# Kernel optimization log

Measured on AMD Instinct MI355X. Metric: run time of the kernel, lower is better.

## Reference

```python
import jax, jax.numpy as jnp
import numpy as np

NUM_BLOCKS_TOTAL = 24  # num_layers(3) * num_blocks(8)
DIL_CYCLE = 8          # dilation = 2 ** (i % 8)


def setup_inputs() -> dict:
    key = jax.random.key(0)
    ks = jax.random.split(key, 12)
    B, C, S, Tq = 256, 32, 32, 256  # batch, residual_ch, skip_ch, queue length
    w = lambda k, sh: jax.random.normal(k, sh, jnp.float32) * 0.1
    return {
        "queues": jax.random.normal(ks[0], (NUM_BLOCKS_TOTAL, B, C, Tq), jnp.float32),
        "x": jax.random.normal(ks[1], (B, 1, 1), jnp.float32),
        "num": jax.random.normal(ks[2], (B, 8, 1), jnp.float32),
        "cat": jax.random.randint(ks[3], (B, 1, 1), 0, 1000),
        "emb_table": w(ks[4], (1000, 16)),
        "W_in": w(ks[5], (C, 25)), "b_in": jnp.zeros((C,), jnp.float32),
        "W_conv": w(ks[6], (NUM_BLOCKS_TOTAL, 2 * C, C, 2)),
        "b_conv": jnp.zeros((NUM_BLOCKS_TOTAL, 2 * C), jnp.float32),
        "W_res": w(ks[7], (NUM_BLOCKS_TOTAL, C, C)),
        "b_res": jnp.zeros((NUM_BLOCKS_TOTAL, C), jnp.float32),
        "W_skip": w(ks[8], (NUM_BLOCKS_TOTAL, S, C)),
        "b_skip": jnp.zeros((NUM_BLOCKS_TOTAL, S), jnp.float32),
        "W_o1": w(ks[9], (128, NUM_BLOCKS_TOTAL * S)), "b_o1": jnp.zeros((128,), jnp.float32),
        "W_o2": w(ks[10], (1, 128)), "b_o2": jnp.zeros((1,), jnp.float32),
    }


def reference(queues, x, num, cat, emb_table, W_in, b_in, W_conv, b_conv,
              W_res, b_res, W_skip, b_skip, W_o1, b_o1, W_o2, b_o2):
    # --- input assembly: concat(x, num, embeds(cat)) along channels, 1 timestep ---
    emb = emb_table[cat[:, 0, 0]][:, :, None]            # [B,16,1]
    inp = jnp.concatenate([x, num, emb], axis=1)          # [B,25,1]
    # pointwise input_conv (kernel_size=1)
    cur = jnp.einsum('oc,bct->bot', W_in, inp) + b_in[None, :, None]  # [B,C,1]

    new_queues = []
    skips = []
    for i in range(NUM_BLOCKS_TOTAL):
        d = 2 ** (i % DIL_CYCLE)
        q = jnp.concatenate([queues[i], cur], axis=2)     # grow queue: [B,C,Tq+1]
        new_queues.append(q)
        # fast_forward: kernel-2 dilated causal conv on last and (last - d) taps
        tap0 = q[:, :, -1 - d]                            # [B,C]
        tap1 = q[:, :, -1]                                # [B,C]
        z = tap0 @ W_conv[i, :, :, 0].T + tap1 @ W_conv[i, :, :, 1].T + b_conv[i]  # [B,2C]
        fz, gz = jnp.split(z, 2, axis=1)
        gated = jnp.tanh(fz) * jax.nn.sigmoid(gz)          # [B,C]
        skips.append(gated @ W_skip[i].T + b_skip[i])      # [B,S]
        cur = (gated @ W_res[i].T + b_res[i] + tap1)[:, :, None]  # residual -> next queue

    sk = jax.nn.relu(jnp.concatenate(skips, axis=1))       # [B, 24*S]
    sk = jax.nn.relu(sk @ W_o1.T + b_o1)                   # [B,128]
    out = (sk @ W_o2.T + b_o2)[:, :, None]                 # [B,1,1]
    return out, jnp.stack(new_queues, axis=0)
```

## Files before the change

### kernel.cpp

```cpp
#include <hip/hip_runtime.h>

#define NBLK 24
#define BATCH 256
#define CCH 32
#define TQ 256
#define TQO 257
#define NCOMP 32
#define BPG 8
#define ROWS_PER_WG 16

__global__ __launch_bounds__(256) void w2w_kernel(
    const float* __restrict__ qin,
    const float* __restrict__ x,
    const float* __restrict__ num,
    const int*   __restrict__ cat,
    const float* __restrict__ emb,
    const float* __restrict__ W_in,  const float* __restrict__ b_in,
    const float* __restrict__ W_conv,const float* __restrict__ b_conv,
    const float* __restrict__ W_res, const float* __restrict__ b_res,
    const float* __restrict__ W_skip,const float* __restrict__ b_skip,
    const float* __restrict__ W_o1,  const float* __restrict__ b_o1,
    const float* __restrict__ W_o2,  const float* __restrict__ b_o2,
    float* __restrict__ out, float* __restrict__ qout)
{
    const int tid = threadIdx.x;

    if (blockIdx.x >= NCOMP) {
        const int wg = blockIdx.x - NCOMP;
        const int row_base = wg * ROWS_PER_WG;
        const int rsub = tid >> 6;
        const int t4   = tid & 63;
        #pragma unroll
        for (int rr = 0; rr < ROWS_PER_WG; rr += 4) {
            const int r = row_base + rr + rsub;
            const float4 v = *(const float4*)(qin + (size_t)r * TQ + t4 * 4);
            float* dst = qout + (size_t)r * TQO + t4 * 4;
            dst[0] = v.x; dst[1] = v.y; dst[2] = v.z; dst[3] = v.w;
        }
        return;
    }

    __shared__ float s_tap[BPG][CCH + 1];
    __shared__ float s_cur[BPG][CCH + 1];
    __shared__ float s_g  [BPG][CCH + 1];
    __shared__ float s_sk [BPG][CCH + 1];

    const int bl = tid >> 5;
    const int j  = tid & 31;
    const int b  = blockIdx.x * BPG + bl;

    float inp[25];
    inp[0] = x[b];
    #pragma unroll
    for (int k = 0; k < 8; ++k) inp[1 + k] = num[b * 8 + k];
    const int ci = cat[b];
    #pragma unroll
    for (int k = 0; k < 16; ++k) inp[9 + k] = emb[ci * 16 + k];

    float cur = b_in[j];
    #pragma unroll
    for (int c = 0; c < 25; ++c) cur = fmaf(W_in[j * 25 + c], inp[c], cur);

    float h0 = 0.f, h1 = 0.f, h2 = 0.f, h3 = 0.f;

    for (int i = 0; i < NBLK; ++i) {
        const int d = 1 << (i & 7);
        const float tap0 = qin[((size_t)(i * BATCH + b) * CCH + j) * TQ + (TQ - d)];

        s_tap[bl][j] = tap0;
        s_cur[bl][j] = cur;
        __syncthreads();

        float z0 = b_conv[i * 2 * CCH + j];
        float z1 = b_conv[i * 2 * CCH + CCH + j];
        const float* wc0 = W_conv + (size_t)(i * 2 * CCH + j)       * CCH * 2;
        const float* wc1 = W_conv + (size_t)(i * 2 * CCH + CCH + j) * CCH * 2;
        #pragma unroll
        for (int c = 0; c < CCH; ++c) {
            const float t0 = s_tap[bl][c];
            const float t1 = s_cur[bl][c];
            z0 = fmaf(t0, wc0[c * 2], z0);
            z0 = fmaf(t1, wc0[c * 2 + 1], z0);
            z1 = fmaf(t0, wc1[c * 2], z1);
            z1 = fmaf(t1, wc1[c * 2 + 1], z1);
        }
        const float g = tanhf(z0) * (1.f / (1.f + __expf(-z1)));

        qout[((size_t)(i * BATCH + b) * CCH + j) * TQO + TQ] = cur;

        s_g[bl][j] = g;
        __syncthreads();

        float sk = b_skip[i * CCH + j];
        float cn = b_res[i * CCH + j] + cur;
        const float* ws = W_skip + (size_t)(i * CCH + j) * CCH;
        const float* wr = W_res  + (size_t)(i * CCH + j) * CCH;
        #pragma unroll
        for (int k = 0; k < CCH; ++k) {
            const float gk = s_g[bl][k];
            sk = fmaf(gk, ws[k], sk);
            cn = fmaf(gk, wr[k], cn);
        }
        s_sk[bl][j] = fmaxf(sk, 0.f);
        cur = cn;
        __syncthreads();

        const float* wo1 = W_o1 + i * CCH;
        #pragma unroll
        for (int s = 0; s < CCH; ++s) {
            const float rs = s_sk[bl][s];
            h0 = fmaf(rs, wo1[(j)      * (NBLK * CCH) + s], h0);
            h1 = fmaf(rs, wo1[(j + 32) * (NBLK * CCH) + s], h1);
            h2 = fmaf(rs, wo1[(j + 64) * (NBLK * CCH) + s], h2);
            h3 = fmaf(rs, wo1[(j + 96) * (NBLK * CCH) + s], h3);
        }
    }

    float p = 0.f;
    p = fmaf(fmaxf(h0 + b_o1[j],      0.f), W_o2[j],      p);
    p = fmaf(fmaxf(h1 + b_o1[j + 32], 0.f), W_o2[j + 32], p);
    p = fmaf(fmaxf(h2 + b_o1[j + 64], 0.f), W_o2[j + 64], p);
    p = fmaf(fmaxf(h3 + b_o1[j + 96], 0.f), W_o2[j + 96], p);
    #pragma unroll
    for (int m = 16; m >= 1; m >>= 1) p += __shfl_xor(p, m);
    if (j == 0) out[b] = p + b_o2[0];
}

extern "C" void kernel_launch(void* const* d_in, const int* in_sizes, int n_in,
                              void* d_out, int out_size, void* d_ws, size_t ws_size,
                              hipStream_t stream) {
    const float* qin    = (const float*)d_in[0];
    const float* x      = (const float*)d_in[1];
    const float* num    = (const float*)d_in[2];
    const int*   cat    = (const int*)  d_in[3];
    const float* emb    = (const float*)d_in[4];
    const float* W_in   = (const float*)d_in[5];
    const float* b_in   = (const float*)d_in[6];
    const float* W_conv = (const float*)d_in[7];
    const float* b_conv = (const float*)d_in[8];
    const float* W_res  = (const float*)d_in[9];
    const float* b_res  = (const float*)d_in[10];
    const float* W_skip = (const float*)d_in[11];
    const float* b_skip = (const float*)d_in[12];
    const float* W_o1   = (const float*)d_in[13];
    const float* b_o1   = (const float*)d_in[14];
    const float* W_o2   = (const float*)d_in[15];
    const float* b_o2   = (const float*)d_in[16];

    float* out  = (float*)d_out;
    float* qout = (float*)d_out + BATCH;

    const int rows  = NBLK * BATCH * CCH;
    const int ncopy = rows / ROWS_PER_WG;
    dim3 grid(NCOMP + ncopy), block(256);
    hipLaunchKernelGGL(w2w_kernel, grid, block, 0, stream,
                       qin, x, num, cat, emb, W_in, b_in, W_conv, b_conv,
                       W_res, b_res, W_skip, b_skip, W_o1, b_o1, W_o2, b_o2,
                       out, qout);
}
```

Measured before the change: 559.0 us.

## Stage per-block weights in LDS with register prefetch and realign queue copy

The compute blocks now prefetch the next layer's conv, residual, skip and output weights into registers and commit them to shared memory, so the FMA loops read vectorized, swizzled LDS instead of strided global loads. Intra-wave barriers replace two of the three block-wide syncs per layer, and the next tap is loaded one layer ahead. The copy path now assigns 16 rows per wave instead of per workgroup, with destination-aligned float4 stores and scalar fixups for edge elements. This raises LDS usage and register pressure, and the copy now uses unaligned vector loads.

```diff
diff --git a/kernel.cpp b/kernel.cpp
--- a/kernel.cpp
+++ b/kernel.cpp
@@ -7,7 +7,11 @@
 #define TQO 257
 #define NCOMP 32
 #define BPG 8
-#define ROWS_PER_WG 16
+#define NCOPY 3072
+#define ROWS (NBLK*BATCH*CCH)
+
+typedef float f4a4  __attribute__((ext_vector_type(4), aligned(4)));
+typedef float f4a16 __attribute__((ext_vector_type(4)));
 
 __global__ __launch_bounds__(256) void w2w_kernel(
     const float* __restrict__ qin,
@@ -23,97 +27,169 @@
     const float* __restrict__ W_o2,  const float* __restrict__ b_o2,
     float* __restrict__ out, float* __restrict__ qout)
 {
+    __shared__ __align__(16) float smem[11264];
     const int tid = threadIdx.x;
 
     if (blockIdx.x >= NCOMP) {
-        const int wg = blockIdx.x - NCOMP;
-        const int row_base = wg * ROWS_PER_WG;
-        const int rsub = tid >> 6;
-        const int t4   = tid & 63;
-        #pragma unroll
-        for (int rr = 0; rr < ROWS_PER_WG; rr += 4) {
-            const int r = row_base + rr + rsub;
-            const float4 v = *(const float4*)(qin + (size_t)r * TQ + t4 * 4);
-            float* dst = qout + (size_t)r * TQO + t4 * 4;
-            dst[0] = v.x; dst[1] = v.y; dst[2] = v.z; dst[3] = v.w;
+        const int wid  = (blockIdx.x - NCOMP) * 4 + (tid >> 6);
+        const int lane = tid & 63;
+        size_t r = (size_t)wid * 16;
+        for (int rr = 0; rr < 16; ++rr, ++r) {
+            const size_t sb = r * TQ, db = r * TQO;
+            const int a = (4 - ((int)r & 3)) & 3;
+            if (lane < 63) {
+                f4a4 v = *(const f4a4*)(qin + sb + a + 4 * lane);
+                *(f4a16*)(qout + db + a + 4 * lane) = v;
+            } else {
+                #pragma unroll
+                for (int e = 0; e < 4; ++e) {
+                    const int f = (e < a) ? e : e + 252;
+                    qout[db + f] = qin[sb + f];
+                }
+            }
         }
         return;
     }
 
-    __shared__ float s_tap[BPG][CCH + 1];
-    __shared__ float s_cur[BPG][CCH + 1];
-    __shared__ float s_g  [BPG][CCH + 1];
-    __shared__ float s_sk [BPG][CCH + 1];
+    float* s_wc = smem;
+    float* s_wr = smem + 4096;
+    float* s_ws = smem + 5120;
+    float* s_wo = smem + 6144;
+    float* s_tc = smem + 10240;
+    float* s_g  = smem + 10752;
+    float* s_sk = smem + 11008;
 
     const int bl = tid >> 5;
     const int j  = tid & 31;
+    const int sw = j & 7;
     const int b  = blockIdx.x * BPG + bl;
 
-    float inp[25];
-    inp[0] = x[b];
-    #pragma unroll
-    for (int k = 0; k < 8; ++k) inp[1 + k] = num[b * 8 + k];
-    const int ci = cat[b];
-    #pragma unroll
-    for (int k = 0; k < 16; ++k) inp[9 + k] = emb[ci * 16 + k];
-
-    float cur = b_in[j];
-    #pragma unroll
-    for (int c = 0; c < 25; ++c) cur = fmaf(W_in[j * 25 + c], inp[c], cur);
+    float cur;
+    {
+        float acc = b_in[j];
+        acc = fmaf(W_in[j * 25 + 0], x[b], acc);
+        #pragma unroll
+        for (int k = 0; k < 8; ++k) acc = fmaf(W_in[j * 25 + 1 + k], num[b * 8 + k], acc);
+        const int ci = cat[b];
+        #pragma unroll
+        for (int k = 0; k < 16; ++k) acc = fmaf(W_in[j * 25 + 9 + k], emb[ci * 16 + k], acc);
+        cur = acc;
+    }
 
     float h0 = 0.f, h1 = 0.f, h2 = 0.f, h3 = 0.f;
+    f4a16 rg[10];
+
+    auto issue = [&](int i) {
+        const float* pc = W_conv + (size_t)i * 4096;
+        #pragma unroll
+        for (int k = 0; k < 4; ++k) rg[k] = *(const f4a16*)(pc + (size_t)(tid + 256 * k) * 4);
+        rg[4] = *(const f4a16*)(W_res  + (size_t)i * 1024 + tid * 4);
+        rg[5] = *(const f4a16*)(W_skip + (size_t)i * 1024 + tid * 4);
+        #pragma unroll
+        for (int k = 0; k < 4; ++k) {
+            const int fi = tid + 256 * k;
+            const int m = fi >> 3, p = fi & 7;
+            rg[6 + k] = *(const f4a16*)(W_o1 + (size_t)m * 768 + (size_t)i * 32 + p * 4);
+        }
+    };
+    auto commit = [&]() {
+        #pragma unroll
+        for (int k = 0; k < 4; ++k) *(f4a16*)(s_wc + (tid + 256 * k) * 4) = rg[k];
+        *(f4a16*)(s_wr + tid * 4) = rg[4];
+        *(f4a16*)(s_ws + tid * 4) = rg[5];
+        #pragma unroll
+        for (int k = 0; k < 4; ++k) *(f4a16*)(s_wo + (tid + 256 * k) * 4) = rg[6 + k];
+    };
+
+    issue(0);
+    {
+        const float t0 = qin[((size_t)b * CCH + j) * TQ + (TQ - 1)];
+        s_tc[bl * 64 + 2 * j]     = t0;
+        s_tc[bl * 64 + 2 * j + 1] = cur;
+    }
+    commit();
+    __syncthreads();
 
     for (int i = 0; i < NBLK; ++i) {
-        const int d = 1 << (i & 7);
-        const float tap0 = qin[((size_t)(i * BATCH + b) * CCH + j) * TQ + (TQ - d)];
-
-        s_tap[bl][j] = tap0;
-        s_cur[bl][j] = cur;
+        if (i + 1 < NBLK) issue(i + 1);
+        float tap_nxt = 0.f;
+        if (i + 1 < NBLK) {
+            const int d = 1 << ((i + 1) & 7);
+            tap_nxt = qin[((size_t)((i + 1) * BATCH + b) * CCH + j) * TQ + (TQ - d)];
+        }
+        const float bc0 = b_conv[i * 64 + j];
+        const float bc1 = b_conv[i * 64 + 32 + j];
+        const float brj = b_res[i * 32 + j];
+        const float bsj = b_skip[i * 32 + j];
+
+        const f4a16* wr0 = (const f4a16*)(s_wc) + j * 16;
+        const f4a16* wr1 = (const f4a16*)(s_wc) + (32 + j) * 16;
+        const f4a16* tcv = (const f4a16*)(s_tc) + bl * 16;
+        float z0a = 0.f, z0b = 0.f, z1a = 0.f, z1b = 0.f;
+        #pragma unroll
+        for (int t = 0; t < 16; ++t) {
+            const int k = (t & 8) | ((t ^ sw) & 7);
+            const f4a16 w0 = wr0[k], w1 = wr1[k], dv = tcv[k];
+            z0a = fmaf(w0.x, dv.x, z0a); z0b = fmaf(w0.y, dv.y, z0b);
+            z0a = fmaf(w0.z, dv.z, z0a); z0b = fmaf(w0.w, dv.w, z0b);
+            z1a = fmaf(w1.x, dv.x, z1a); z1b = fmaf(w1.y, dv.y, z1b);
+            z1a = fmaf(w1.z, dv.z, z1a); z1b = fmaf(w1.w, dv.w, z1b);
+        }
+        const float z0 = z0a + z0b + bc0;
+        const float z1 = z1a + z1b + bc1;
+        const float g  = tanhf(z0) * (1.f / (1.f + __expf(-z1)));
+
+        qout[((size_t)(i * BATCH + b) * CCH + j) * TQO + TQ] = cur;
+
+        s_g[bl * 32 + j] = g;
+        __builtin_amdgcn_wave_barrier();
+
+        const f4a16* gv  = (const f4a16*)(s_g)  + bl * 8;
+        const f4a16* wsv = (const f4a16*)(s_ws) + j * 8;
+        const f4a16* wrv = (const f4a16*)(s_wr) + j * 8;
+        float ska = bsj, skb = 0.f, cna = brj + cur, cnb = 0.f;
+        #pragma unroll
+        for (int t = 0; t < 8; ++t) {
+            const int k = (t ^ sw) & 7;
+            const f4a16 gk = gv[k], wv = wsv[k], rv = wrv[k];
+            ska = fmaf(gk.x, wv.x, ska); skb = fmaf(gk.y, wv.y, skb);
+            ska = fmaf(gk.z, wv.z, ska); skb = fmaf(gk.w, wv.w, skb);
+            cna = fmaf(gk.x, rv.x, cna); cnb = fmaf(gk.y, rv.y, cnb);
+            cna = fmaf(gk.z, rv.z, cna); cnb = fmaf(gk.w, rv.w, cnb);
+        }
+        const float skr = fmaxf(ska + skb, 0.f);
+        cur = cna + cnb;
+
+        s_sk[bl * 32 + j] = skr;
+        if (i + 1 < NBLK) {
+            s_tc[bl * 64 + 2 * j]     = tap_nxt;
+            s_tc[bl * 64 + 2 * j + 1] = cur;
+        }
+        __builtin_amdgcn_wave_barrier();
+
+        const f4a16* skv = (const f4a16*)(s_sk) + bl * 8;
+        const f4a16* o0 = (const f4a16*)(s_wo) + j * 8;
+        const f4a16* o1 = (const f4a16*)(s_wo) + (32 + j) * 8;
+        const f4a16* o2 = (const f4a16*)(s_wo) + (64 + j) * 8;
+        const f4a16* o3 = (const f4a16*)(s_wo) + (96 + j) * 8;
+        #pragma unroll
+        for (int t = 0; t < 8; ++t) {
+            const int k = (t ^ sw) & 7;
+            const f4a16 rv = skv[k];
+            const f4a16 a0 = o0[k], a1 = o1[k], a2 = o2[k], a3 = o3[k];
+            h0 = fmaf(rv.x, a0.x, h0); h0 = fmaf(rv.y, a0.y, h0);
+            h0 = fmaf(rv.z, a0.z, h0); h0 = fmaf(rv.w, a0.w, h0);
+            h1 = fmaf(rv.x, a1.x, h1); h1 = fmaf(rv.y, a1.y, h1);
+            h1 = fmaf(rv.z, a1.z, h1); h1 = fmaf(rv.w, a1.w, h1);
+            h2 = fmaf(rv.x, a2.x, h2); h2 = fmaf(rv.y, a2.y, h2);
+            h2 = fmaf(rv.z, a2.z, h2); h2 = fmaf(rv.w, a2.w, h2);
+            h3 = fmaf(rv.x, a3.x, h3); h3 = fmaf(rv.y, a3.y, h3);
+            h3 = fmaf(rv.z, a3.z, h3); h3 = fmaf(rv.w, a3.w, h3);
+        }
+
         __syncthreads();
-
-        float z0 = b_conv[i * 2 * CCH + j];
-        float z1 = b_conv[i * 2 * CCH + CCH + j];
-        const float* wc0 = W_conv + (size_t)(i * 2 * CCH + j)       * CCH * 2;
-        const float* wc1 = W_conv + (size_t)(i * 2 * CCH + CCH + j) * CCH * 2;
-        #pragma unroll
-        for (int c = 0; c < CCH; ++c) {
-            const float t0 = s_tap[bl][c];
-            const float t1 = s_cur[bl][c];
-            z0 = fmaf(t0, wc0[c * 2], z0);
-            z0 = fmaf(t1, wc0[c * 2 + 1], z0);
-            z1 = fmaf(t0, wc1[c * 2], z1);
-            z1 = fmaf(t1, wc1[c * 2 + 1], z1);
-        }
-        const float g = tanhf(z0) * (1.f / (1.f + __expf(-z1)));
-
-        qout[((size_t)(i * BATCH + b) * CCH + j) * TQO + TQ] = cur;
-
-        s_g[bl][j] = g;
+        if (i + 1 < NBLK) commit();
         __syncthreads();
-
-        float sk = b_skip[i * CCH + j];
-        float cn = b_res[i * CCH + j] + cur;
-        const float* ws = W_skip + (size_t)(i * CCH + j) * CCH;
-        const float* wr = W_res  + (size_t)(i * CCH + j) * CCH;
-        #pragma unroll
-        for (int k = 0; k < CCH; ++k) {
-            const float gk = s_g[bl][k];
-            sk = fmaf(gk, ws[k], sk);
-            cn = fmaf(gk, wr[k], cn);
-        }
-        s_sk[bl][j] = fmaxf(sk, 0.f);
-        cur = cn;
-        __syncthreads();
-
-        const float* wo1 = W_o1 + i * CCH;
-        #pragma unroll
-        for (int s = 0; s < CCH; ++s) {
-            const float rs = s_sk[bl][s];
-            h0 = fmaf(rs, wo1[(j)      * (NBLK * CCH) + s], h0);
-            h1 = fmaf(rs, wo1[(j + 32) * (NBLK * CCH) + s], h1);
-            h2 = fmaf(rs, wo1[(j + 64) * (NBLK * CCH) + s], h2);
-            h3 = fmaf(rs, wo1[(j + 96) * (NBLK * CCH) + s], h3);
-        }
     }
 
     float p = 0.f;
@@ -150,9 +226,7 @@
     float* out  = (float*)d_out;
     float* qout = (float*)d_out + BATCH;
 
-    const int rows  = NBLK * BATCH * CCH;
-    const int ncopy = rows / ROWS_PER_WG;
-    dim3 grid(NCOMP + ncopy), block(256);
+    dim3 grid(NCOMP + NCOPY), block(256);
     hipLaunchKernelGGL(w2w_kernel, grid, block, 0, stream,
                        qin, x, num, cat, emb, W_in, b_in, W_conv, b_conv,
                        W_res, b_res, W_skip, b_skip, W_o1, b_o1, W_o2, b_o2,
```

Result: faster. 501.2 us (-10.3%).
